# Kernel tuning notes

Hardware: AMD Instinct MI355X
Metric: run time of the kernel (lower is better)

Reference implementation:

```python
import jax, jax.numpy as jnp
import numpy as np

T, B, S = 12, 65536, 1024       # time steps, total pedestrians, scenes
P = B // S                      # peds per scene (uniform segments)
H_DIM = 64                      # enc_h_dim
D = 4 * H_DIM                   # 256 = concat(h_fwd,h_rev,c_fwd,c_rev)
MLP = 32                        # mlp_dim (obs_enc_feat width)
ZS = 32                         # zS_dim


def setup_inputs() -> dict:
    key = jax.random.key(0)
    ks = jax.random.split(key, 16)
    sc = 1.0 / np.sqrt(H_DIM)
    G = 4 * H_DIM  # gate width (i,f,g,o)
    starts = jnp.arange(S, dtype=jnp.int32) * P
    seq_start_end = jnp.stack([starts, starts + P], axis=1)
    return {
        "last_obs_traj": jax.random.normal(ks[0], (B, 6), jnp.float32),
        "fut_rel_traj": jax.random.normal(ks[1], (T, B, 2), jnp.float32),
        "seq_start_end": seq_start_end,
        "obs_enc_feat": jax.random.normal(ks[2], (B, MLP), jnp.float32),
        "fut_obst": jnp.zeros((T, S, 1), jnp.float32),  # unused by forward
        # initial_h_model / initial_c_model (Linear 6 -> H_DIM)
        "w_h0": jax.random.normal(ks[3], (6, H_DIM), jnp.float32) * sc,
        "b_h0": jnp.zeros((H_DIM,), jnp.float32),
        "w_c0": jax.random.normal(ks[4], (6, H_DIM), jnp.float32) * sc,
        "b_c0": jnp.zeros((H_DIM,), jnp.float32),
        # bidirectional LSTM (input 2, hidden H_DIM), gate order i,f,g,o
        "w_ih_f": jax.random.normal(ks[5], (2, G), jnp.float32) * sc,
        "w_hh_f": jax.random.normal(ks[6], (H_DIM, G), jnp.float32) * sc,
        "b_f": jnp.zeros((G,), jnp.float32),
        "w_ih_r": jax.random.normal(ks[7], (2, G), jnp.float32) * sc,
        "w_hh_r": jax.random.normal(ks[8], (H_DIM, G), jnp.float32) * sc,
        "b_r": jnp.zeros((G,), jnp.float32),
        # fc2: Linear(4h + 4h + mlp_dim -> zS_dim)
        "w_fc2": jax.random.normal(ks[9], (2 * D + MLP, ZS), jnp.float32) * 0.05,
        "b_fc2": jnp.zeros((ZS,), jnp.float32),
    }


def _lstm_scan(xs, h0, c0, w_ih, w_hh, b):
    """Run an LSTM over xs (T,B,in); return final (h, c). Gate order i,f,g,o."""
    def step(carry, x):
        h, c = carry
        z = x @ w_ih + h @ w_hh + b
        i, f, g, o = jnp.split(z, 4, axis=-1)
        c = jax.nn.sigmoid(f) * c + jax.nn.sigmoid(i) * jnp.tanh(g)
        h = jax.nn.sigmoid(o) * jnp.tanh(c)
        return (h, c), None
    (hT, cT), _ = jax.lax.scan(step, (h0, c0), xs)
    return hT, cT


def reference(last_obs_traj, fut_rel_traj, seq_start_end, obs_enc_feat, fut_obst,
              w_h0, b_h0, w_c0, b_c0,
              w_ih_f, w_hh_f, b_f, w_ih_r, w_hh_r, b_r,
              w_fc2, b_fc2):
    # initial states: forward direction from linear maps, reverse direction zeros
    h0_f = last_obs_traj @ w_h0 + b_h0
    c0_f = last_obs_traj @ w_c0 + b_c0
    zeros = jnp.zeros_like(h0_f)

    hf, cf = _lstm_scan(fut_rel_traj, h0_f, c0_f, w_ih_f, w_hh_f, b_f)
    hr, cr = _lstm_scan(fut_rel_traj[::-1], zeros, zeros, w_ih_r, w_hh_r, b_r)

    # torch: state = cat((h_n, c_n), dim=0).permute(1,0,2).reshape(B, 4h)
    final_encoder_h = jnp.concatenate([hf, hr, cf, cr], axis=1)  # (B, 256)

    # per-scene softmax attention pooling: context = softmax(H H^T) @ H
    n_scenes = seq_start_end.shape[0]
    Hs = final_encoder_h.reshape(n_scenes, -1, final_encoder_h.shape[1])  # (S,P,D)
    attn = jax.nn.softmax(jnp.einsum('spd,sqd->spq', Hs, Hs), axis=-1)
    pool_h = jnp.einsum('spq,sqd->spd', attn, Hs).reshape(final_encoder_h.shape)

    dist_fc_input = jnp.concatenate([final_encoder_h, pool_h, obs_enc_feat], axis=1)
    stats = dist_fc_input @ w_fc2 + b_fc2
    return dist_fc_input, stats
```

## Files before the change

### kernel.cpp

```cpp
#include <hip/hip_runtime.h>

#define T_STEPS 12
#define NPED 65536
#define NSCENE 1024
#define PSC 64
#define HID 64
#define DDIM 256
#define DIST 544
#define ZS 32

typedef unsigned int u32;
typedef unsigned short u16;
typedef __attribute__((ext_vector_type(8))) short bf16x8;
typedef __attribute__((ext_vector_type(4))) float f32x4;

__device__ __forceinline__ float u2f(u32 u) { union { u32 i; float f; } v; v.i = u; return v.f; }
__device__ __forceinline__ u32 f2u(float f) { union { float f; u32 i; } v; v.f = f; return v.i; }
__device__ __forceinline__ float bf2f(u16 u) { return u2f(((u32)u) << 16); }
__device__ __forceinline__ u16 f2bf(float f) {
  u32 i = f2u(f);
  return (u16)((i + 0x7fffu + ((i >> 16) & 1u)) >> 16);
}
__device__ __forceinline__ u32 pack2(float a, float b) { return (u32)f2bf(a) | (((u32)f2bf(b)) << 16); }

__device__ __forceinline__ float fsig(float x) { return __builtin_amdgcn_rcpf(1.0f + __expf(-x)); }
__device__ __forceinline__ float ftanh(float x) {
  float e = __expf(fminf(fmaxf(2.0f * x, -80.0f), 80.0f));
  return (e - 1.0f) * __builtin_amdgcn_rcpf(e + 1.0f);
}
__device__ __forceinline__ void unpack8(const uint4 v, float* f) {
  f[0] = u2f(v.x << 16); f[1] = u2f(v.x & 0xffff0000u);
  f[2] = u2f(v.y << 16); f[3] = u2f(v.y & 0xffff0000u);
  f[4] = u2f(v.z << 16); f[5] = u2f(v.z & 0xffff0000u);
  f[6] = u2f(v.w << 16); f[7] = u2f(v.w & 0xffff0000u);
}

__device__ __forceinline__ bool inputs_are_bf16(const u16* probe) {
  const int lane = threadIdx.x & 63;
  const u16 w = probe[2 * lane];
  const u32 e = (w >> 7) & 0xffu;
  const bool ok = (w == 0) || (e >= 96u && e <= 144u);
  return __popcll(__ballot(ok)) >= 48;
}

template<bool FP32>
__device__ __forceinline__ float ld(const void* p, int idx) {
  if (FP32) return ((const float*)p)[idx];
  return bf2f(((const u16*)p)[idx]);
}
template<bool FP32>
__device__ __forceinline__ void ld8(const void* p, size_t idx8, float* f) {
  if (FP32) {
    const float4 a = ((const float4*)p)[idx8 >> 2];
    const float4 b = ((const float4*)p)[(idx8 >> 2) + 1];
    f[0] = a.x; f[1] = a.y; f[2] = a.z; f[3] = a.w;
    f[4] = b.x; f[5] = b.y; f[6] = b.z; f[7] = b.w;
  } else {
    unpack8(((const uint4*)p)[idx8 >> 3], f);
  }
}
template<bool FP32>
__device__ __forceinline__ void ldpair(const void* p, size_t pairidx, float& a, float& b) {
  if (FP32) {
    const float2 v = ((const float2*)p)[pairidx];
    a = v.x; b = v.y;
  } else {
    const u32 xx = ((const u32*)p)[pairidx];
    a = u2f(xx << 16); b = u2f(xx & 0xffff0000u);
  }
}
template<bool FP32>
__device__ __forceinline__ void st8(void* p, size_t idx8, const float* f) {
  if (FP32) {
    float4 a; a.x = f[0]; a.y = f[1]; a.z = f[2]; a.w = f[3];
    float4 b; b.x = f[4]; b.y = f[5]; b.z = f[6]; b.w = f[7];
    ((float4*)p)[idx8 >> 2] = a;
    ((float4*)p)[(idx8 >> 2) + 1] = b;
  } else {
    uint4 pk;
    pk.x = pack2(f[0], f[1]); pk.y = pack2(f[2], f[3]);
    pk.z = pack2(f[4], f[5]); pk.w = pack2(f[6], f[7]);
    ((uint4*)p)[idx8 >> 3] = pk;
  }
}
template<bool FP32>
__device__ __forceinline__ void st4(void* p, size_t idx4, const float4 v) {
  if (FP32) {
    ((float4*)p)[idx4 >> 2] = v;
  } else {
    uint2 pk; pk.x = pack2(v.x, v.y); pk.y = pack2(v.z, v.w);
    *(uint2*)((u16*)p + idx4) = pk;
  }
}

template<bool FP32>
__device__ __forceinline__ void lstm_body(
    const void* __restrict__ last_obs, const void* __restrict__ fut,
    const void* __restrict__ w_h0, const void* __restrict__ b_h0,
    const void* __restrict__ w_c0, const void* __restrict__ b_c0,
    const void* __restrict__ w_ih_f, const void* __restrict__ w_hh_f, const void* __restrict__ b_gf,
    const void* __restrict__ w_ih_r, const void* __restrict__ w_hh_r, const void* __restrict__ b_gr,
    void* __restrict__ outv,
    u16* __restrict__ wTp, u16* __restrict__ wXp, u16* __restrict__ hbp)
{
  const int tid  = threadIdx.x;
  const int wave = tid >> 6;
  const int lane = tid & 63;
  const int l15  = lane & 15;
  const int lhi  = lane >> 4;
  const int ped0 = blockIdx.x * 64 + wave * 16;
  const int xm   = (lane & 7) << 4;
  const int e0   = (lhi * 16) ^ xm;
  const int e1   = (64 + lhi * 16) ^ xm;
  const int foff0 = l15 * 128 + e0;
  const int foff1 = l15 * 128 + e1;
  char* const hw = (char*)hbp + wave * 2048;
  char* const wb = (char*)wTp;
  char* const wxrow = (char*)wXp + l15 * 128;

  float c[16];

  for (int dir = 0; dir < 2; ++dir) {
    const void* whh = dir ? w_hh_r : w_hh_f;
    const void* wih = dir ? w_ih_r : w_ih_f;
    const void* bg  = dir ? b_gr  : b_gf;

    __syncthreads();
    #pragma unroll
    for (int c8 = 0; c8 < 8; ++c8) {
      const int n = tid, k0 = c8 * 8;
      u32 pk[4];
      #pragma unroll
      for (int h = 0; h < 4; ++h) {
        u16 ea, eb;
        if (FP32) {
          ea = f2bf(((const float*)whh)[(k0 + 2 * h) * DDIM + n]);
          eb = f2bf(((const float*)whh)[(k0 + 2 * h + 1) * DDIM + n]);
        } else {
          ea = ((const u16*)whh)[(k0 + 2 * h) * DDIM + n];
          eb = ((const u16*)whh)[(k0 + 2 * h + 1) * DDIM + n];
        }
        pk[h] = (u32)ea | ((u32)eb << 16);
      }
      uint4 v; v.x = pk[0]; v.y = pk[1]; v.z = pk[2]; v.w = pk[3];
      *(uint4*)(wb + n * 128 + ((k0 * 2) ^ ((n & 7) << 4))) = v;
    }
    {
      const int tg2 = tid >> 4, col = tid & 15;
      const float wi0 = ld<FP32>(wih, tg2 * 16 + col);
      const float wi1 = ld<FP32>(wih, DDIM + tg2 * 16 + col);
      const float bb  = ld<FP32>(bg,  tg2 * 16 + col);
      char* const wx = (char*)wXp;
      const int base = (tg2 >> 1) * 2048 + col * 128;
      const int kofs = (tg2 & 1) * 64;
      const int swz  = (col & 7) << 4;
      uint4 v0; v0.x = pack2(wi0, wi1); v0.y = (u32)f2bf(bb); v0.z = 0u; v0.w = 0u;
      uint4 zz; zz.x = 0u; zz.y = 0u; zz.z = 0u; zz.w = 0u;
      *(uint4*)(wx + base + ((kofs +  0) ^ swz)) = v0;
      *(uint4*)(wx + base + ((kofs + 16) ^ swz)) = zz;
      *(uint4*)(wx + base + ((kofs + 32) ^ swz)) = zz;
      *(uint4*)(wx + base + ((kofs + 48) ^ swz)) = zz;
    }

    if (dir == 0) {
      float xo[4][6];
      #pragma unroll
      for (int r = 0; r < 4; ++r)
        #pragma unroll
        for (int k = 0; k < 6; ++k)
          xo[r][k] = ld<FP32>(last_obs, (ped0 + lhi * 4 + r) * 6 + k);
      #pragma unroll
      for (int jj = 0; jj < 4; ++jj) {
        const int j = jj * 16 + l15;
        float wh[6], wc[6];
        #pragma unroll
        for (int k = 0; k < 6; ++k) {
          wh[k] = ld<FP32>(w_h0, k * HID + j);
          wc[k] = ld<FP32>(w_c0, k * HID + j);
        }
        const float bh = ld<FP32>(b_h0, j), bc = ld<FP32>(b_c0, j);
        #pragma unroll
        for (int r = 0; r < 4; ++r) {
          float h0 = bh, c0 = bc;
          #pragma unroll
          for (int k = 0; k < 6; ++k) {
            h0 = fmaf(xo[r][k], wh[k], h0);
            c0 = fmaf(xo[r][k], wc[k], c0);
          }
          c[jj * 4 + r] = c0;
          const int p = lhi * 4 + r;
          *(u16*)(hw + p * 128 + ((j * 2) ^ ((p & 7) << 4))) = f2bf(h0);
        }
      }
    } else {
      #pragma unroll
      for (int jj = 0; jj < 4; ++jj) {
        const int j = jj * 16 + l15;
        #pragma unroll
        for (int r = 0; r < 4; ++r) {
          c[jj * 4 + r] = 0.0f;
          const int p = lhi * 4 + r;
          *(u16*)(hw + p * 128 + ((j * 2) ^ ((p & 7) << 4))) = 0;
        }
      }
    }
    __syncthreads();

    for (int t = 0; t < T_STEPS; ++t) {
      const int tt = dir ? (T_STEPS - 1 - t) : t;
      float xa, xb2;
      ldpair<FP32>(fut, (size_t)tt * NPED + ped0 + l15, xa, xb2);
      union { bf16x8 v; u32 w[4]; } ax;
      ax.w[0] = (lhi == 0) ? pack2(xa, xb2) : 0u;
      ax.w[1] = (lhi == 0) ? 0x00003f80u : 0u;
      ax.w[2] = 0u; ax.w[3] = 0u;

      __asm__ volatile("" ::: "memory");
      const bf16x8 a0 = *(const bf16x8*)(hw + foff0);
      const bf16x8 a1 = *(const bf16x8*)(hw + foff1);

      f32x4 acc[16];
      #pragma unroll
      for (int tg = 0; tg < 16; ++tg) {
        const bf16x8 bx = *(const bf16x8*)(wxrow + (tg >> 1) * 2048 + ((tg & 1) ? e1 : e0));
        const bf16x8 b0 = *(const bf16x8*)(wb + tg * 2048 + foff0);
        const bf16x8 b1 = *(const bf16x8*)(wb + tg * 2048 + foff1);
        f32x4 z = {0.0f, 0.0f, 0.0f, 0.0f};
        z = __builtin_amdgcn_mfma_f32_16x16x32_bf16(ax.v, bx, z, 0, 0, 0);
        z = __builtin_amdgcn_mfma_f32_16x16x32_bf16(a0, b0, z, 0, 0, 0);
        acc[tg] = __builtin_amdgcn_mfma_f32_16x16x32_bf16(a1, b1, z, 0, 0, 0);
      }
      __asm__ volatile("" ::: "memory");

      #pragma unroll
      for (int jj = 0; jj < 4; ++jj) {
        const int j = jj * 16 + l15;
        #pragma unroll
        for (int r = 0; r < 4; ++r) {
          const float ig = fsig(acc[jj][r]);
          const float fg = fsig(acc[jj + 4][r]);
          const float gg = ftanh(acc[jj + 8][r]);
          const float og = fsig(acc[jj + 12][r]);
          const float cn = fmaf(fg, c[jj * 4 + r], ig * gg);
          c[jj * 4 + r] = cn;
          const float hn = og * ftanh(cn);
          const int p = lhi * 4 + r;
          *(u16*)(hw + p * 128 + ((j * 2) ^ ((p & 7) << 4))) = f2bf(hn);
        }
      }
      __asm__ volatile("" ::: "memory");
    }

    __syncthreads();
    float* const tb = (float*)wTp + wave * 1024;
    #pragma unroll
    for (int jj = 0; jj < 4; ++jj)
      #pragma unroll
      for (int r = 0; r < 4; ++r)
        tb[(lhi * 4 + r) * 64 + jj * 16 + l15] = c[jj * 4 + r];
    __asm__ volatile("" ::: "memory");
    #pragma unroll
    for (int r = 0; r < 4; ++r) {
      const int pl = r * 4 + lhi;
      const u32* hp = (const u32*)(hw + pl * 128 + ((l15 * 8) ^ ((pl & 7) << 4)));
      const u32 h01 = hp[0], h23 = hp[1];
      float4 hv;
      hv.x = u2f(h01 << 16); hv.y = u2f(h01 & 0xffff0000u);
      hv.z = u2f(h23 << 16); hv.w = u2f(h23 & 0xffff0000u);
      const float4 cv = *(const float4*)&tb[pl * 64 + l15 * 4];
      const size_t rb = (size_t)(ped0 + pl) * DIST;
      st4<FP32>(outv, rb + (dir ? 64 : 0) + l15 * 4, hv);
      st4<FP32>(outv, rb + 128 + (dir ? 64 : 0) + l15 * 4, cv);
    }
  }
}

__global__ __launch_bounds__(256, 2)
void lstm_kernel(const void* last_obs, const void* fut,
                 const void* w_h0, const void* b_h0,
                 const void* w_c0, const void* b_c0,
                 const void* w_ih_f, const void* w_hh_f, const void* b_gf,
                 const void* w_ih_r, const void* w_hh_r, const void* b_gr,
                 void* outv)
{
  __shared__ __align__(16) u16 wT[DDIM * HID];
  __shared__ __align__(16) u16 wX[8 * 1024];
  __shared__ __align__(16) u16 hb[4][16 * HID];
  if (inputs_are_bf16((const u16*)fut))
    lstm_body<false>(last_obs, fut, w_h0, b_h0, w_c0, b_c0,
                     w_ih_f, w_hh_f, b_gf, w_ih_r, w_hh_r, b_gr, outv, wT, wX, &hb[0][0]);
  else
    lstm_body<true>(last_obs, fut, w_h0, b_h0, w_c0, b_c0,
                    w_ih_f, w_hh_f, b_gf, w_ih_r, w_hh_r, b_gr, outv, wT, wX, &hb[0][0]);
}

template<bool FP32>
__device__ __forceinline__ void pool_body(
    const void* __restrict__ obs, const void* __restrict__ wfc,
    const void* __restrict__ bfc, void* __restrict__ outv,
    u16* __restrict__ Hrow, u16* __restrict__ Breg)
{
  const int tid  = threadIdx.x;
  const int wave = tid >> 6;
  const int lane = tid & 63;
  const int l15  = lane & 15;
  const int lhi  = lane >> 4;
  const int pedbase = blockIdx.x * PSC;
  const int wbase = wave * 16;
  char* const hb = (char*)Hrow;
  char* const tr = (char*)Breg;
  char* const pb = (char*)Breg + 32768;
  const int swl = (l15 & 7) << 4;

  if (FP32) {
    const float* ob = (const float*)outv;
    for (int i = tid; i < PSC * 64; i += 256) {
      const int pp = i >> 6, dd = (i & 63) << 2;
      const float4 v = *(const float4*)(ob + (size_t)(pedbase + pp) * DIST + dd);
      uint2 w; w.x = pack2(v.x, v.y); w.y = pack2(v.z, v.w);
      *(uint2*)(hb + pp * 512 + ((2 * dd) ^ ((pp & 7) << 4))) = w;
    }
  } else {
    const u16* ob = (const u16*)outv;
    for (int i = tid; i < PSC * 32; i += 256) {
      const int pp = i >> 5, dd = (i & 31) << 3;
      *(uint4*)(hb + pp * 512 + ((2 * dd) ^ ((pp & 7) << 4))) =
          *(const uint4*)(ob + (size_t)(pedbase + pp) * DIST + dd);
    }
  }
  __syncthreads();

  {
    const int p = tid >> 2, q4 = tid & 3;
    const int swp = (p & 7) << 4;
    #pragma unroll
    for (int j = 0; j < 8; ++j) {
      const int d0 = q4 * 64 + j * 8;
      const uint4 v = *(const uint4*)(hb + p * 512 + ((2 * d0) ^ swp));
      const u16* e = (const u16*)&v;
      #pragma unroll
      for (int jj = 0; jj < 8; ++jj) {
        const int d = d0 + jj;
        *(u16*)(tr + d * 128 + ((2 * p) ^ ((d & 7) << 4))) = e[jj];
      }
    }
  }

  f32x4 acc[4];
  #pragma unroll
  for (int b = 0; b < 4; ++b) acc[b] = (f32x4){0.0f, 0.0f, 0.0f, 0.0f};
  for (int kt = 0; kt < 8; ++kt) {
    const int ko = kt * 64 + lhi * 16;
    const bf16x8 af = *(const bf16x8*)(hb + (wbase + l15) * 512 + (ko ^ swl));
    #pragma unroll
    for (int b = 0; b < 4; ++b) {
      const bf16x8 bf = *(const bf16x8*)(hb + (b * 16 + l15) * 512 + (ko ^ swl));
      acc[b] = __builtin_amdgcn_mfma_f32_16x16x32_bf16(af, bf, acc[b], 0, 0, 0);
    }
  }

  float P[4][4];
  #pragma unroll
  for (int r = 0; r < 4; ++r) {
    float mx = fmaxf(fmaxf(acc[0][r], acc[1][r]), fmaxf(acc[2][r], acc[3][r]));
    mx = fmaxf(mx, __shfl_xor(mx, 1));
    mx = fmaxf(mx, __shfl_xor(mx, 2));
    mx = fmaxf(mx, __shfl_xor(mx, 4));
    mx = fmaxf(mx, __shfl_xor(mx, 8));
    float s = 0.0f;
    #pragma unroll
    for (int b = 0; b < 4; ++b) { P[b][r] = __expf(acc[b][r] - mx); s += P[b][r]; }
    s += __shfl_xor(s, 1); s += __shfl_xor(s, 2);
    s += __shfl_xor(s, 4); s += __shfl_xor(s, 8);
    const float inv = __builtin_amdgcn_rcpf(s);
    #pragma unroll
    for (int b = 0; b < 4; ++b) P[b][r] *= inv;
  }

  #pragma unroll
  for (int b = 0; b < 4; ++b)
    #pragma unroll
    for (int r = 0; r < 4; ++r) {
      const int p = wbase + lhi * 4 + r, q = b * 16 + l15;
      *(u16*)(pb + p * 128 + ((2 * q) ^ ((p & 7) << 4))) = f2bf(P[b][r]);
    }
  __syncthreads();

  const bf16x8 pa0 = *(const bf16x8*)(pb + (wbase + l15) * 128 + ((     lhi * 16) ^ swl));
  const bf16x8 pa1 = *(const bf16x8*)(pb + (wbase + l15) * 128 + ((64 + lhi * 16) ^ swl));
  float* const stgp = (float*)(pb + wave * 2048);
  bf16x8 pf[8];
  #pragma unroll
  for (int e = 0; e < 8; ++e) {
    f32x4 pv[2];
    #pragma unroll
    for (int n = 0; n < 2; ++n) {
      const int d = e * 32 + n * 16 + l15;
      const int swd = (d & 7) << 4;
      const bf16x8 b0 = *(const bf16x8*)(tr + d * 128 + ((     lhi * 16) ^ swd));
      const bf16x8 b1 = *(const bf16x8*)(tr + d * 128 + ((64 + lhi * 16) ^ swd));
      f32x4 z = {0.0f, 0.0f, 0.0f, 0.0f};
      z = __builtin_amdgcn_mfma_f32_16x16x32_bf16(pa0, b0, z, 0, 0, 0);
      pv[n] = __builtin_amdgcn_mfma_f32_16x16x32_bf16(pa1, b1, z, 0, 0, 0);
    }
    __asm__ volatile("" ::: "memory");
    #pragma unroll
    for (int n = 0; n < 2; ++n)
      #pragma unroll
      for (int r = 0; r < 4; ++r)
        stgp[(lhi * 4 + r) * 32 + n * 16 + l15] = pv[n][r];
    __asm__ volatile("" ::: "memory");
    #pragma unroll
    for (int s = 0; s < 2; ++s) {
      const int idx = lane * 2 + s;
      const int pl = idx >> 3, q = idx & 7;
      const float4 v = *(const float4*)&stgp[pl * 32 + q * 4];
      st4<FP32>(outv, (size_t)(pedbase + wbase + pl) * DIST + DDIM + e * 32 + q * 4, v);
    }
    {
      const float4 a = *(const float4*)&stgp[l15 * 32 + lhi * 8];
      const float4 b = *(const float4*)&stgp[l15 * 32 + lhi * 8 + 4];
      union { bf16x8 v; uint4 u; } fr;
      fr.u.x = pack2(a.x, a.y); fr.u.y = pack2(a.z, a.w);
      fr.u.z = pack2(b.x, b.y); fr.u.w = pack2(b.z, b.w);
      pf[e] = fr.v;
    }
    __asm__ volatile("" ::: "memory");
  }

  bf16x8 of;
  {
    const int p = tid >> 2, part = tid & 3;
    float ov[8];
    ld8<FP32>(obs, (size_t)(pedbase + p) * ZS + part * 8, ov);
    st8<FP32>(outv, (size_t)(pedbase + p) * DIST + 2 * DDIM + part * 8, ov);
    float om[8];
    ld8<FP32>(obs, (size_t)(pedbase + wbase + l15) * ZS + lhi * 8, om);
    union { bf16x8 v; uint4 u; } fr;
    fr.u.x = pack2(om[0], om[1]); fr.u.y = pack2(om[2], om[3]);
    fr.u.z = pack2(om[4], om[5]); fr.u.w = pack2(om[6], om[7]);
    of = fr.v;
  }

  __syncthreads();

  for (int i = tid; i < DIST * ZS; i += 256) {
    const int k = i >> 5, z = i & 31;
    const u16 w = FP32 ? f2bf(((const float*)wfc)[i]) : ((const u16*)wfc)[i];
    *(u16*)(tr + (k >> 5) * 2048 + z * 64 + ((2 * (k & 31)) ^ ((z & 3) << 4))) = w;
  }
  __syncthreads();

  {
    f32x4 s0 = {0.0f, 0.0f, 0.0f, 0.0f}, s1 = {0.0f, 0.0f, 0.0f, 0.0f};
    const int bofs = (lhi * 16) ^ ((l15 & 3) << 4);
    #pragma unroll
    for (int kt = 0; kt < 17; ++kt) {
      bf16x8 av;
      if (kt < 8) {
        const int ko = kt * 64 + lhi * 16;
        av = *(const bf16x8*)(hb + (wbase + l15) * 512 + (ko ^ swl));
      } else if (kt < 16) {
        av = pf[kt - 8];
      } else {
        av = of;
      }
      const char* wfb = tr + kt * 2048;
      const bf16x8 b0 = *(const bf16x8*)(wfb + (l15     ) * 64 + bofs);
      const bf16x8 b1 = *(const bf16x8*)(wfb + (l15 + 16) * 64 + bofs);
      s0 = __builtin_amdgcn_mfma_f32_16x16x32_bf16(av, b0, s0, 0, 0, 0);
      s1 = __builtin_amdgcn_mfma_f32_16x16x32_bf16(av, b1, s1, 0, 0, 0);
    }
    const float bb0 = ld<FP32>(bfc, l15), bb1 = ld<FP32>(bfc, 16 + l15);
    float* const stgh = (float*)(hb + wave * 8192);
    __asm__ volatile("" ::: "memory");
    #pragma unroll
    for (int r = 0; r < 4; ++r) {
      stgh[(lhi * 4 + r) * 32 + l15     ] = s0[r] + bb0;
      stgh[(lhi * 4 + r) * 32 + l15 + 16] = s1[r] + bb1;
    }
    __asm__ volatile("" ::: "memory");
    #pragma unroll
    for (int s = 0; s < 2; ++s) {
      const int idx = lane * 2 + s;
      const int pl = idx >> 3, q = idx & 7;
      const float4 v = *(const float4*)&stgh[pl * 32 + q * 4];
      st4<FP32>(outv, (size_t)NPED * DIST + (size_t)(pedbase + wbase + pl) * ZS + q * 4, v);
    }
  }
}

__global__ __launch_bounds__(256, 2)
void pool_kernel(const void* fut, const void* obs, const void* wfc,
                 const void* bfc, void* outv)
{
  __shared__ __align__(16) u16 Hrow[PSC * DDIM];
  __shared__ __align__(16) u16 Breg[20480];
  if (inputs_are_bf16((const u16*)fut)) pool_body<false>(obs, wfc, bfc, outv, Hrow, Breg);
  else                                  pool_body<true>(obs, wfc, bfc, outv, Hrow, Breg);
}

extern "C" void kernel_launch(void* const* d_in, const int* in_sizes, int n_in,
                              void* d_out, int out_size, void* d_ws, size_t ws_size,
                              hipStream_t stream) {
  const void* last_obs = d_in[0];
  const void* fut      = d_in[1];
  const void* obs      = d_in[3];
  const void* w_h0  = d_in[5];
  const void* b_h0  = d_in[6];
  const void* w_c0  = d_in[7];
  const void* b_c0  = d_in[8];
  const void* w_ih_f = d_in[9];
  const void* w_hh_f = d_in[10];
  const void* b_f    = d_in[11];
  const void* w_ih_r = d_in[12];
  const void* w_hh_r = d_in[13];
  const void* b_r    = d_in[14];
  const void* w_fc2  = d_in[15];
  const void* b_fc2  = d_in[16];

  lstm_kernel<<<dim3(NPED / 64), dim3(256), 0, stream>>>(
      last_obs, fut, w_h0, b_h0, w_c0, b_c0,
      w_ih_f, w_hh_f, b_f, w_ih_r, w_hh_r, b_r, d_out);
  pool_kernel<<<dim3(NSCENE), dim3(256), 0, stream>>>(fut, obs, w_fc2, b_fc2, d_out);
}
```

Baseline: 387.4 us.

## Fuse LSTM encoder and scene attention pooling into one kernel

Merges the LSTM kernel and the per-scene pooling/fc2 kernel into one launch, with one block per scene. Final h/c states go straight from registers into a shared-memory row buffer, so the pooling stage no longer re-reads them from global memory, and one launch boundary goes away. The input-weight tile is also compacted, with a single shared zero vector serving the upper lanes. The cost is a larger shared-memory footprint (~78KB) that may limit occupancy, plus region aliasing whose correctness depends on the barriers between stages.

```diff
diff --git a/kernel.cpp b/kernel.cpp
--- a/kernel.cpp
+++ b/kernel.cpp
@@ -8,6 +8,13 @@
 #define DDIM 256
 #define DIST 544
 #define ZS 32
+
+#define SM_BYTES 78336
+#define WT_OFF   0
+#define WX_OFF   32768
+#define WXZ_OFF  36864
+#define HB_OFF   36992
+#define HROW_OFF 45568
 
 typedef unsigned int u32;
 typedef unsigned short u16;
@@ -94,29 +101,34 @@
 }
 
 template<bool FP32>
-__device__ __forceinline__ void lstm_body(
+__device__ __forceinline__ void enc_body(
     const void* __restrict__ last_obs, const void* __restrict__ fut,
     const void* __restrict__ w_h0, const void* __restrict__ b_h0,
     const void* __restrict__ w_c0, const void* __restrict__ b_c0,
     const void* __restrict__ w_ih_f, const void* __restrict__ w_hh_f, const void* __restrict__ b_gf,
     const void* __restrict__ w_ih_r, const void* __restrict__ w_hh_r, const void* __restrict__ b_gr,
-    void* __restrict__ outv,
-    u16* __restrict__ wTp, u16* __restrict__ wXp, u16* __restrict__ hbp)
+    const void* __restrict__ obs, const void* __restrict__ wfc,
+    const void* __restrict__ bfc, void* __restrict__ outv,
+    char* __restrict__ SM)
 {
   const int tid  = threadIdx.x;
   const int wave = tid >> 6;
   const int lane = tid & 63;
   const int l15  = lane & 15;
   const int lhi  = lane >> 4;
-  const int ped0 = blockIdx.x * 64 + wave * 16;
+  const int pedbase = blockIdx.x * 64;
+  const int ped0 = pedbase + wave * 16;
+  const int wbase = wave * 16;
   const int xm   = (lane & 7) << 4;
   const int e0   = (lhi * 16) ^ xm;
   const int e1   = (64 + lhi * 16) ^ xm;
   const int foff0 = l15 * 128 + e0;
   const int foff1 = l15 * 128 + e1;
-  char* const hw = (char*)hbp + wave * 2048;
-  char* const wb = (char*)wTp;
-  char* const wxrow = (char*)wXp + l15 * 128;
+  const int swl  = (l15 & 7) << 4;
+  char* const hw = SM + HB_OFF + wave * 2048;
+  char* const wb = SM + WT_OFF;
+  char* const wx = SM + WX_OFF;
+  char* const hrow = SM + HROW_OFF;
 
   float c[16];
 
@@ -150,16 +162,12 @@
       const float wi0 = ld<FP32>(wih, tg2 * 16 + col);
       const float wi1 = ld<FP32>(wih, DDIM + tg2 * 16 + col);
       const float bb  = ld<FP32>(bg,  tg2 * 16 + col);
-      char* const wx = (char*)wXp;
-      const int base = (tg2 >> 1) * 2048 + col * 128;
-      const int kofs = (tg2 & 1) * 64;
-      const int swz  = (col & 7) << 4;
       uint4 v0; v0.x = pack2(wi0, wi1); v0.y = (u32)f2bf(bb); v0.z = 0u; v0.w = 0u;
-      uint4 zz; zz.x = 0u; zz.y = 0u; zz.z = 0u; zz.w = 0u;
-      *(uint4*)(wx + base + ((kofs +  0) ^ swz)) = v0;
-      *(uint4*)(wx + base + ((kofs + 16) ^ swz)) = zz;
-      *(uint4*)(wx + base + ((kofs + 32) ^ swz)) = zz;
-      *(uint4*)(wx + base + ((kofs + 48) ^ swz)) = zz;
+      *(uint4*)(wx + tg2 * 256 + col * 16) = v0;
+      if (tid == 0) {
+        uint4 zz; zz.x = 0u; zz.y = 0u; zz.z = 0u; zz.w = 0u;
+        *(uint4*)(SM + WXZ_OFF) = zz;
+      }
     }
 
     if (dir == 0) {
@@ -222,7 +230,8 @@
       f32x4 acc[16];
       #pragma unroll
       for (int tg = 0; tg < 16; ++tg) {
-        const bf16x8 bx = *(const bf16x8*)(wxrow + (tg >> 1) * 2048 + ((tg & 1) ? e1 : e0));
+        const char* bxa = (lhi == 0) ? (wx + tg * 256 + l15 * 16) : (SM + WXZ_OFF);
+        const bf16x8 bx = *(const bf16x8*)bxa;
         const bf16x8 b0 = *(const bf16x8*)(wb + tg * 2048 + foff0);
         const bf16x8 b1 = *(const bf16x8*)(wb + tg * 2048 + foff1);
         f32x4 z = {0.0f, 0.0f, 0.0f, 0.0f};
@@ -252,7 +261,7 @@
     }
 
     __syncthreads();
-    float* const tb = (float*)wTp + wave * 1024;
+    float* const tb = (float*)(SM + WT_OFF) + wave * 1024;
     #pragma unroll
     for (int jj = 0; jj < 4; ++jj)
       #pragma unroll
@@ -271,64 +280,19 @@
       const size_t rb = (size_t)(ped0 + pl) * DIST;
       st4<FP32>(outv, rb + (dir ? 64 : 0) + l15 * 4, hv);
       st4<FP32>(outv, rb + 128 + (dir ? 64 : 0) + l15 * 4, cv);
-    }
-  }
-}
-
-__global__ __launch_bounds__(256, 2)
-void lstm_kernel(const void* last_obs, const void* fut,
-                 const void* w_h0, const void* b_h0,
-                 const void* w_c0, const void* b_c0,
-                 const void* w_ih_f, const void* w_hh_f, const void* b_gf,
-                 const void* w_ih_r, const void* w_hh_r, const void* b_gr,
-                 void* outv)
-{
-  __shared__ __align__(16) u16 wT[DDIM * HID];
-  __shared__ __align__(16) u16 wX[8 * 1024];
-  __shared__ __align__(16) u16 hb[4][16 * HID];
-  if (inputs_are_bf16((const u16*)fut))
-    lstm_body<false>(last_obs, fut, w_h0, b_h0, w_c0, b_c0,
-                     w_ih_f, w_hh_f, b_gf, w_ih_r, w_hh_r, b_gr, outv, wT, wX, &hb[0][0]);
-  else
-    lstm_body<true>(last_obs, fut, w_h0, b_h0, w_c0, b_c0,
-                    w_ih_f, w_hh_f, b_gf, w_ih_r, w_hh_r, b_gr, outv, wT, wX, &hb[0][0]);
-}
-
-template<bool FP32>
-__device__ __forceinline__ void pool_body(
-    const void* __restrict__ obs, const void* __restrict__ wfc,
-    const void* __restrict__ bfc, void* __restrict__ outv,
-    u16* __restrict__ Hrow, u16* __restrict__ Breg)
-{
-  const int tid  = threadIdx.x;
-  const int wave = tid >> 6;
-  const int lane = tid & 63;
-  const int l15  = lane & 15;
-  const int lhi  = lane >> 4;
-  const int pedbase = blockIdx.x * PSC;
-  const int wbase = wave * 16;
-  char* const hb = (char*)Hrow;
-  char* const tr = (char*)Breg;
-  char* const pb = (char*)Breg + 32768;
-  const int swl = (l15 & 7) << 4;
-
-  if (FP32) {
-    const float* ob = (const float*)outv;
-    for (int i = tid; i < PSC * 64; i += 256) {
-      const int pp = i >> 6, dd = (i & 63) << 2;
-      const float4 v = *(const float4*)(ob + (size_t)(pedbase + pp) * DIST + dd);
-      uint2 w; w.x = pack2(v.x, v.y); w.y = pack2(v.z, v.w);
-      *(uint2*)(hb + pp * 512 + ((2 * dd) ^ ((pp & 7) << 4))) = w;
-    }
-  } else {
-    const u16* ob = (const u16*)outv;
-    for (int i = tid; i < PSC * 32; i += 256) {
-      const int pp = i >> 5, dd = (i & 31) << 3;
-      *(uint4*)(hb + pp * 512 + ((2 * dd) ^ ((pp & 7) << 4))) =
-          *(const uint4*)(ob + (size_t)(pedbase + pp) * DIST + dd);
+      const int p = wbase + pl;
+      const int psw = (p & 7) << 4;
+      const int hd = (dir ? 64 : 0) + l15 * 4;
+      uint2 hw2; hw2.x = pack2(hv.x, hv.y); hw2.y = pack2(hv.z, hv.w);
+      uint2 cw2; cw2.x = pack2(cv.x, cv.y); cw2.y = pack2(cv.z, cv.w);
+      *(uint2*)(hrow + p * 512 + ((2 * hd) ^ psw)) = hw2;
+      *(uint2*)(hrow + p * 512 + ((2 * (128 + hd)) ^ psw)) = cw2;
     }
   }
   __syncthreads();
+
+  char* const tr = SM + WT_OFF;
+  char* const pb = SM + HB_OFF;
 
   {
     const int p = tid >> 2, q4 = tid & 3;
@@ -336,7 +300,7 @@
     #pragma unroll
     for (int j = 0; j < 8; ++j) {
       const int d0 = q4 * 64 + j * 8;
-      const uint4 v = *(const uint4*)(hb + p * 512 + ((2 * d0) ^ swp));
+      const uint4 v = *(const uint4*)(hrow + p * 512 + ((2 * d0) ^ swp));
       const u16* e = (const u16*)&v;
       #pragma unroll
       for (int jj = 0; jj < 8; ++jj) {
@@ -351,10 +315,10 @@
   for (int b = 0; b < 4; ++b) acc[b] = (f32x4){0.0f, 0.0f, 0.0f, 0.0f};
   for (int kt = 0; kt < 8; ++kt) {
     const int ko = kt * 64 + lhi * 16;
-    const bf16x8 af = *(const bf16x8*)(hb + (wbase + l15) * 512 + (ko ^ swl));
+    const bf16x8 af = *(const bf16x8*)(hrow + (wbase + l15) * 512 + (ko ^ swl));
     #pragma unroll
     for (int b = 0; b < 4; ++b) {
-      const bf16x8 bf = *(const bf16x8*)(hb + (b * 16 + l15) * 512 + (ko ^ swl));
+      const bf16x8 bf = *(const bf16x8*)(hrow + (b * 16 + l15) * 512 + (ko ^ swl));
       acc[b] = __builtin_amdgcn_mfma_f32_16x16x32_bf16(af, bf, acc[b], 0, 0, 0);
     }
   }
@@ -459,7 +423,7 @@
       bf16x8 av;
       if (kt < 8) {
         const int ko = kt * 64 + lhi * 16;
-        av = *(const bf16x8*)(hb + (wbase + l15) * 512 + (ko ^ swl));
+        av = *(const bf16x8*)(hrow + (wbase + l15) * 512 + (ko ^ swl));
       } else if (kt < 16) {
         av = pf[kt - 8];
       } else {
@@ -472,7 +436,7 @@
       s1 = __builtin_amdgcn_mfma_f32_16x16x32_bf16(av, b1, s1, 0, 0, 0);
     }
     const float bb0 = ld<FP32>(bfc, l15), bb1 = ld<FP32>(bfc, 16 + l15);
-    float* const stgh = (float*)(hb + wave * 8192);
+    float* const stgh = (float*)(hrow + wave * 8192);
     __asm__ volatile("" ::: "memory");
     #pragma unroll
     for (int r = 0; r < 4; ++r) {
@@ -491,13 +455,23 @@
 }
 
 __global__ __launch_bounds__(256, 2)
-void pool_kernel(const void* fut, const void* obs, const void* wfc,
-                 const void* bfc, void* outv)
+void enc_kernel(const void* last_obs, const void* fut,
+                const void* w_h0, const void* b_h0,
+                const void* w_c0, const void* b_c0,
+                const void* w_ih_f, const void* w_hh_f, const void* b_gf,
+                const void* w_ih_r, const void* w_hh_r, const void* b_gr,
+                const void* obs, const void* wfc, const void* bfc,
+                void* outv)
 {
-  __shared__ __align__(16) u16 Hrow[PSC * DDIM];
-  __shared__ __align__(16) u16 Breg[20480];
-  if (inputs_are_bf16((const u16*)fut)) pool_body<false>(obs, wfc, bfc, outv, Hrow, Breg);
-  else                                  pool_body<true>(obs, wfc, bfc, outv, Hrow, Breg);
+  __shared__ __align__(16) char SM[SM_BYTES];
+  if (inputs_are_bf16((const u16*)fut))
+    enc_body<false>(last_obs, fut, w_h0, b_h0, w_c0, b_c0,
+                    w_ih_f, w_hh_f, b_gf, w_ih_r, w_hh_r, b_gr,
+                    obs, wfc, bfc, outv, SM);
+  else
+    enc_body<true>(last_obs, fut, w_h0, b_h0, w_c0, b_c0,
+                   w_ih_f, w_hh_f, b_gf, w_ih_r, w_hh_r, b_gr,
+                   obs, wfc, bfc, outv, SM);
 }
 
 extern "C" void kernel_launch(void* const* d_in, const int* in_sizes, int n_in,
@@ -519,8 +493,8 @@
   const void* w_fc2  = d_in[15];
   const void* b_fc2  = d_in[16];
 
-  lstm_kernel<<<dim3(NPED / 64), dim3(256), 0, stream>>>(
+  enc_kernel<<<dim3(NSCENE), dim3(256), 0, stream>>>(
       last_obs, fut, w_h0, b_h0, w_c0, b_c0,
-      w_ih_f, w_hh_f, b_f, w_ih_r, w_hh_r, b_r, d_out);
-  pool_kernel<<<dim3(NSCENE), dim3(256), 0, stream>>>(fut, obs, w_fc2, b_fc2, d_out);
-}
+      w_ih_f, w_hh_f, b_f, w_ih_r, w_hh_r, b_r,
+      obs, w_fc2, b_fc2, d_out);
+}
```

After: 365.6 us. 1.06x faster.
